# Performance work log

Measured on AMD Instinct MI355X. Metric: run time of the kernel, lower is better.

The kernel has to match this reference:

```python
import jax, jax.numpy as jnp
import numpy as np

B, P, D, A = 256, 196, 512, 512

def setup_inputs() -> dict:
    key = jax.random.key(0)
    ks = jax.random.split(key, 12)
    sc = 1.0 / np.sqrt(D)
    sa = 1.0 / np.sqrt(A)
    return {
        "encoder_out": jax.random.normal(ks[0], (B, P, D), jnp.float32),
        "decoder_hidden": jax.random.normal(ks[1], (B, D), jnp.float32),
        "st": jax.random.normal(ks[2], (B, D), jnp.float32),
        "Wv": jax.random.normal(ks[3], (D, A), jnp.float32) * sc,
        "bv": jnp.zeros((A,), jnp.float32),
        "Wh": jax.random.normal(ks[4], (D, A), jnp.float32) * sc,
        "bh": jnp.zeros((A,), jnp.float32),
        "Ws": jax.random.normal(ks[5], (D, A), jnp.float32) * sc,
        "bs": jnp.zeros((A,), jnp.float32),
        "Wav": jax.random.normal(ks[6], (A,), jnp.float32) * sa,
        "bav": jnp.zeros((), jnp.float32),
        "Was": jax.random.normal(ks[7], (A,), jnp.float32) * sa,
        "bas": jnp.zeros((), jnp.float32),
    }

def reference(encoder_out, decoder_hidden, st, Wv, bv, Wh, bh, Ws, bs, Wav, bav, Was, bas):
    # hidden: (B, A)
    hidden = decoder_hidden @ Wh + bh
    # v: (B, P, A)
    v = jnp.einsum('bpd,da->bpa', encoder_out, Wv) + bv
    # z_t: (B, P) -- additive attention scores over pixels
    z_t = jnp.einsum('bpa,a->bp', jnp.tanh(v + hidden[:, None, :]), Wav) + bav
    alpha_t = jax.nn.softmax(z_t, axis=1)
    # c_t: (B, D) -- attention-weighted encoding
    c_t = jnp.einsum('bpd,bp->bd', encoder_out, alpha_t)
    # sentinel branch: s (B, A), s_att (B, 1)
    s = st @ Ws + bs
    s_att = jnp.tanh(s + hidden) @ Was + bas  # (B,)
    z_t_extended = jnp.concatenate([z_t, s_att[:, None]], axis=1)  # (B, P+1)
    alpha_t_hat = jax.nn.softmax(z_t_extended, axis=1)
    beta_t = alpha_t_hat[:, -1:]  # (B, 1)
    c_hat_t = beta_t * st + (1.0 - beta_t) * c_t
    return (c_hat_t, alpha_t, beta_t)
```

## Files before the change

### kernel.cpp

```cpp
#include <hip/hip_runtime.h>
#include <hip/hip_bf16.h>
#include <cstdint>

#define B_ 256
#define P_ 196
#define D_ 512
#define A_ 512

#define OUT_CHAT  0
#define OUT_ALPHA (B_*D_)
#define OUT_BETA  (B_*D_ + B_*P_)

typedef unsigned short ushort_t;
typedef uint32_t u32;
typedef uint64_t u64;
typedef __attribute__((ext_vector_type(8))) __bf16 bf16x8;
typedef __attribute__((ext_vector_type(4))) float f32x4;

__device__ __forceinline__ ushort_t f2bf(float f) {
    union { float f; u32 i; } v; v.f = f;
    u32 r = (v.i + 0x7fffu + ((v.i >> 16) & 1u)) >> 16;
    return (ushort_t)r;
}
__device__ __forceinline__ u32 cvt2bf(float x, float y) {
    union { __hip_bfloat162 h; u32 u; } v;
    v.h = __float22bfloat162_rn(make_float2(x, y));
    return v.u;
}
__device__ __forceinline__ float tanh_fast(float x) {
    float e = __expf(2.0f * x);
    return 1.0f - 2.0f / (e + 1.0f);
}

__global__ __launch_bounds__(256) void k0_transpose(
    const float* __restrict__ W, ushort_t* __restrict__ WT)
{
    __shared__ ushort_t tile[32][33];
    int bx = blockIdx.x, by = blockIdx.y;
    int t = threadIdx.x, r = t >> 5, c = t & 31;
#pragma unroll
    for (int i = 0; i < 4; ++i) {
        int row = r + 8 * i;
        tile[row][c] = f2bf(W[(size_t)(by * 32 + row) * A_ + bx * 32 + c]);
    }
    __syncthreads();
#pragma unroll
    for (int i = 0; i < 4; ++i) {
        int row = r + 8 * i;
        WT[(size_t)(bx * 32 + row) * D_ + by * 32 + c] = tile[c][row];
    }
}

__global__ __launch_bounds__(256) void kcvt_small(
    const float* __restrict__ dh, const float* __restrict__ st,
    ushort_t* __restrict__ dhbf, ushort_t* __restrict__ stbf,
    float* __restrict__ z_ws, float* __restrict__ ct_ws)
{
    int gid = blockIdx.x * 256 + threadIdx.x;
    const float4* dsrc = (const float4*)dh;
    const float4* ssrc = (const float4*)st;
    float4 dv = dsrc[gid], sv = ssrc[gid];
    ((u64*)dhbf)[gid] = (u64)cvt2bf(dv.x, dv.y) | ((u64)cvt2bf(dv.z, dv.w) << 32);
    ((u64*)stbf)[gid] = (u64)cvt2bf(sv.x, sv.y) | ((u64)cvt2bf(sv.z, sv.w) << 32);
    ((float4*)ct_ws)[gid] = (float4){0.f, 0.f, 0.f, 0.f};
    z_ws[gid < B_ * P_ ? gid : 0] = 0.f;
    if (gid < B_ * P_ - 32768) z_ws[gid + 32768] = 0.f;
}

__global__ __launch_bounds__(256) void kE_cvt(
    const float* __restrict__ E, ushort_t* __restrict__ Ebf)
{
    size_t i0 = (size_t)blockIdx.x * 512 + threadIdx.x;
    const float4* src = (const float4*)E;
    u64* dst = (u64*)Ebf;
    float4 v0 = src[i0];
    float4 v1 = src[i0 + 256];
    u64 p0 = (u64)cvt2bf(v0.x, v0.y) | ((u64)cvt2bf(v0.z, v0.w) << 32);
    u64 p1 = (u64)cvt2bf(v1.x, v1.y) | ((u64)cvt2bf(v1.z, v1.w) << 32);
    dst[i0]       = p0;
    dst[i0 + 256] = p1;
}

#define PADK 72

__global__ __launch_bounds__(256) void k1_mfma(
    const ushort_t* __restrict__ dhbf, const ushort_t* __restrict__ stbf,
    const ushort_t* __restrict__ WhT,  const ushort_t* __restrict__ WsT,
    const float* __restrict__ bh, const float* __restrict__ bs,
    float* __restrict__ hidden_ws, float* __restrict__ s_ws)
{
    __shared__ ushort_t As[128 * PADK];
    __shared__ ushort_t Bs[128 * PADK];

    int mat = blockIdx.z;
    const ushort_t* Abf = mat ? stbf : dhbf;
    const ushort_t* WT  = mat ? WsT  : WhT;
    const float*    bia = mat ? bs   : bh;
    float*          outp = mat ? s_ws : hidden_ws;

    int tid = threadIdx.x;
    int m0 = blockIdx.y * 128;
    int n0 = blockIdx.x * 128;

    int lane = tid & 63, w = tid >> 6;
    int wm = w & 1, wn = w >> 1;
    int col = lane & 15, q = lane >> 4;

    f32x4 acc[4][4];
#pragma unroll
    for (int tm = 0; tm < 4; ++tm)
#pragma unroll
        for (int tn = 0; tn < 4; ++tn)
            acc[tm][tn] = (f32x4){0.f, 0.f, 0.f, 0.f};

    const ushort_t* arow = As + (wm * 64 + col) * PADK + q * 8;
    const ushort_t* brow = Bs + (wn * 64 + col) * PADK + q * 8;

    int sr = tid >> 3, sc = tid & 7;
    for (int kt = 0; kt < D_ / 64; ++kt) {
#pragma unroll
        for (int i = 0; i < 4; ++i) {
            int row = sr + i * 32;
            *(uint4*)(As + row * PADK + sc * 8) =
                *(const uint4*)(Abf + (size_t)(m0 + row) * D_ + kt * 64 + sc * 8);
            *(uint4*)(Bs + row * PADK + sc * 8) =
                *(const uint4*)(WT + (size_t)(n0 + row) * D_ + kt * 64 + sc * 8);
        }
        __syncthreads();
#pragma unroll
        for (int ks = 0; ks < 2; ++ks) {
            bf16x8 afr[4];
#pragma unroll
            for (int tm = 0; tm < 4; ++tm)
                afr[tm] = *(const bf16x8*)(arow + tm * 16 * PADK + ks * 32);
#pragma unroll
            for (int tn = 0; tn < 4; ++tn) {
                bf16x8 bfr = *(const bf16x8*)(brow + tn * 16 * PADK + ks * 32);
#pragma unroll
                for (int tm = 0; tm < 4; ++tm)
                    acc[tm][tn] = __builtin_amdgcn_mfma_f32_16x16x32_bf16(
                        afr[tm], bfr, acc[tm][tn], 0, 0, 0);
            }
        }
        __syncthreads();
    }

#pragma unroll
    for (int tm = 0; tm < 4; ++tm)
#pragma unroll
        for (int r = 0; r < 4; ++r) {
            int b = m0 + wm * 64 + tm * 16 + q * 4 + r;
#pragma unroll
            for (int tn = 0; tn < 4; ++tn) {
                int n = n0 + wn * 64 + tn * 16 + col;
                outp[(size_t)b * A_ + n] = acc[tm][tn][r] + bia[n];
            }
        }
}

#define BM 128
#define BN 256
#define BKk 64
__global__ __launch_bounds__(256, 2) void k2_z_bf(
    const ushort_t* __restrict__ Ebf, const ushort_t* __restrict__ WvT,
    const float* __restrict__ hidden_ws, const float* __restrict__ bv,
    const float* __restrict__ Wav, float* __restrict__ z_ws)
{
    __shared__ ushort_t As[BM * PADK];
    __shared__ ushort_t Bs[BN * PADK];
    __shared__ float hv_s[2][BN];
    __shared__ float wav_s[BN];
    __shared__ float zpart[2][BM];

    int tid = threadIdx.x;
    int m0  = blockIdx.x * BM;
    int n0  = blockIdx.y * BN;
    int b0  = m0 / P_;
    int b1  = (m0 + BM - 1) / P_;

    {
        int a = n0 + tid;
        float bva = bv[a];
        hv_s[0][tid] = hidden_ws[(size_t)b0 * A_ + a] + bva;
        hv_s[1][tid] = hidden_ws[(size_t)b1 * A_ + a] + bva;
        wav_s[tid]   = Wav[a];
    }

    int lane = tid & 63, w = tid >> 6;
    int wm = w & 1, wn = w >> 1;
    int col = lane & 15, q = lane >> 4;

    f32x4 acc[4][8];
#pragma unroll
    for (int tm = 0; tm < 4; ++tm)
#pragma unroll
        for (int tn = 0; tn < 8; ++tn)
            acc[tm][tn] = (f32x4){0.f, 0.f, 0.f, 0.f};

    const ushort_t* arow = As + (wm * 64 + col) * PADK + q * 8;
    const ushort_t* brow = Bs + (wn * 128 + col) * PADK + q * 8;

    int sr = tid >> 3, sc = tid & 7;

    for (int kt = 0; kt < D_ / BKk; ++kt) {
#pragma unroll
        for (int i = 0; i < 4; ++i) {
            int row = sr + i * 32;
            *(uint4*)(As + row * PADK + sc * 8) =
                *(const uint4*)(Ebf + (size_t)(m0 + row) * D_ + kt * BKk + sc * 8);
        }
#pragma unroll
        for (int i = 0; i < 8; ++i) {
            int row = sr + i * 32;
            *(uint4*)(Bs + row * PADK + sc * 8) =
                *(const uint4*)(WvT + (size_t)(n0 + row) * D_ + kt * BKk + sc * 8);
        }
        __syncthreads();
#pragma unroll
        for (int ks = 0; ks < 2; ++ks) {
            bf16x8 afr[4], bfr[8];
#pragma unroll
            for (int tm = 0; tm < 4; ++tm)
                afr[tm] = *(const bf16x8*)(arow + tm * 16 * PADK + ks * 32);
#pragma unroll
            for (int tn = 0; tn < 8; ++tn)
                bfr[tn] = *(const bf16x8*)(brow + tn * 16 * PADK + ks * 32);
#pragma unroll
            for (int tm = 0; tm < 4; ++tm)
#pragma unroll
                for (int tn = 0; tn < 8; ++tn)
                    acc[tm][tn] = __builtin_amdgcn_mfma_f32_16x16x32_bf16(
                        afr[tm], bfr[tn], acc[tm][tn], 0, 0, 0);
        }
        __syncthreads();
    }

#pragma unroll
    for (int tm = 0; tm < 4; ++tm) {
#pragma unroll
        for (int r = 0; r < 4; ++r) {
            int row = wm * 64 + tm * 16 + q * 4 + r;
            int m   = m0 + row;
            int bsel = (m / P_) - b0;
            float zr = 0.f;
#pragma unroll
            for (int tn = 0; tn < 8; ++tn) {
                int nl = wn * 128 + tn * 16 + col;
                zr += wav_s[nl] * tanh_fast(acc[tm][tn][r] + hv_s[bsel][nl]);
            }
#pragma unroll
            for (int msk = 1; msk < 16; msk <<= 1)
                zr += __shfl_xor(zr, msk, 64);
            if (col == 0) zpart[wn][row] = zr;
        }
    }
    __syncthreads();
    if (tid < BM) {
        int m = m0 + tid;
        int b = m / P_;
        int p = m - b * P_;
        atomicAdd(&z_ws[(size_t)b * P_ + p], zpart[0][tid] + zpart[1][tid]);
    }
}

__global__ __launch_bounds__(256) void k3_softmax(
    const float* __restrict__ z_ws, const float* __restrict__ hidden_ws,
    const float* __restrict__ s_ws, const float* __restrict__ Was,
    const float* __restrict__ bas, const float* __restrict__ bav,
    float* __restrict__ alpha_ws, float* __restrict__ beta_ws,
    float* __restrict__ out)
{
    __shared__ float red[4];
    __shared__ float bm_s, bl_s, sa_s;
    int b = blockIdx.x, t = threadIdx.x;

    {
        int a0 = t, a1 = t + 256;
        float part = Was[a0] * tanh_fast(s_ws[(size_t)b * A_ + a0] + hidden_ws[(size_t)b * A_ + a0])
                   + Was[a1] * tanh_fast(s_ws[(size_t)b * A_ + a1] + hidden_ws[(size_t)b * A_ + a1]);
#pragma unroll
        for (int o = 32; o >= 1; o >>= 1) part += __shfl_down(part, o, 64);
        if ((t & 63) == 0) red[t >> 6] = part;
        __syncthreads();
        if (t == 0) sa_s = red[0] + red[1] + red[2] + red[3] + bas[0];
        __syncthreads();
    }

    float zv = (t < P_) ? (z_ws[(size_t)b * P_ + t] + bav[0]) : -1e30f;

    float m = zv;
#pragma unroll
    for (int o = 32; o >= 1; o >>= 1) m = fmaxf(m, __shfl_xor(m, o, 64));
    if ((t & 63) == 0) red[t >> 6] = m;
    __syncthreads();
    if (t == 0) bm_s = fmaxf(fmaxf(red[0], red[1]), fmaxf(red[2], red[3]));
    __syncthreads();
    float m1 = bm_s;

    float e = (t < P_) ? __expf(zv - m1) : 0.f;
    float s = e;
#pragma unroll
    for (int o = 32; o >= 1; o >>= 1) s += __shfl_xor(s, o, 64);
    if ((t & 63) == 0) red[t >> 6] = s;
    __syncthreads();
    if (t == 0) bl_s = red[0] + red[1] + red[2] + red[3];
    __syncthreads();
    float l1 = bl_s;

    if (t < P_) {
        float alpha = e / l1;
        alpha_ws[(size_t)b * P_ + t] = alpha;
        out[OUT_ALPHA + (size_t)b * P_ + t] = alpha;
    }
    float sa = sa_s;
    float m2 = fmaxf(m1, sa);
    float l2 = __expf(m1 - m2) * l1 + __expf(sa - m2);
    float beta = __expf(sa - m2) / l2;
    if (t == 0) {
        beta_ws[b] = beta;
        out[OUT_BETA + b] = beta;
    }
}

#define PCH 49
__global__ __launch_bounds__(256) void k4_ct_partial(
    const float* __restrict__ E, const float* __restrict__ alpha_ws,
    float* __restrict__ ct_ws)
{
    __shared__ float al[PCH];
    int b = blockIdx.x, pc = blockIdx.y, t = threadIdx.x;
    int pbase = pc * PCH;
    if (t < PCH) al[t] = alpha_ws[(size_t)b * P_ + pbase + t];
    __syncthreads();
    const float* eb = E + ((size_t)b * P_ + pbase) * D_ + 2 * t;
    float a0 = 0.f, a1 = 0.f;
#pragma unroll 7
    for (int p = 0; p < PCH; ++p) {
        float2 u = *(const float2*)(eb + (size_t)p * D_);
        float ap = al[p];
        a0 = fmaf(ap, u.x, a0);
        a1 = fmaf(ap, u.y, a1);
    }
    atomicAdd(&ct_ws[(size_t)b * D_ + 2 * t],     a0);
    atomicAdd(&ct_ws[(size_t)b * D_ + 2 * t + 1], a1);
}

__global__ __launch_bounds__(256) void k4_combine(
    const float* __restrict__ st, const float* __restrict__ ct_ws,
    const float* __restrict__ beta_ws, float* __restrict__ out)
{
    int b = blockIdx.x, t = threadIdx.x;
    float beta = beta_ws[b];
    float2 su = *(const float2*)(st + (size_t)b * D_ + 2 * t);
    float2 cu = *(const float2*)(ct_ws + (size_t)b * D_ + 2 * t);
    float c0 = beta * su.x + (1.f - beta) * cu.x;
    float c1 = beta * su.y + (1.f - beta) * cu.y;
    *(float2*)(out + (size_t)b * D_ + 2 * t) = make_float2(c0, c1);
}

extern "C" void kernel_launch(void* const* d_in, const int* in_sizes, int n_in,
                              void* d_out, int out_size, void* d_ws, size_t ws_size,
                              hipStream_t stream)
{
    (void)in_sizes; (void)n_in; (void)out_size; (void)ws_size;
    const float* E   = (const float*)d_in[0];
    const float* dh  = (const float*)d_in[1];
    const float* st  = (const float*)d_in[2];
    const float* Wv  = (const float*)d_in[3];
    const float* bv  = (const float*)d_in[4];
    const float* Wh  = (const float*)d_in[5];
    const float* bh  = (const float*)d_in[6];
    const float* Ws  = (const float*)d_in[7];
    const float* bs  = (const float*)d_in[8];
    const float* Wav = (const float*)d_in[9];
    const float* bav = (const float*)d_in[10];
    const float* Was = (const float*)d_in[11];
    const float* bas = (const float*)d_in[12];
    float* out = (float*)d_out;

    char* ws = (char*)d_ws;
    ushort_t* WvT      = (ushort_t*)(ws);
    ushort_t* WhT      = (ushort_t*)(ws + 524288);
    ushort_t* WsT      = (ushort_t*)(ws + 1048576);
    float*    hidden_w = (float*)(ws + 1572864);
    float*    s_w      = (float*)(ws + 2097152);
    float*    z_w      = (float*)(ws + 2621440);
    float*    alpha_w  = (float*)(ws + 2822144);
    float*    beta_w   = (float*)(ws + 3022848);
    float*    ct_w     = (float*)(ws + 3023872);
    ushort_t* dhbf     = (ushort_t*)(ws + 3548160);
    ushort_t* stbf     = (ushort_t*)(ws + 3810304);
    ushort_t* Ebf      = (ushort_t*)(ws + 4072448);

    k0_transpose<<<dim3(16, 16), 256, 0, stream>>>(Wv, WvT);
    k0_transpose<<<dim3(16, 16), 256, 0, stream>>>(Wh, WhT);
    k0_transpose<<<dim3(16, 16), 256, 0, stream>>>(Ws, WsT);
    kcvt_small<<<128, 256, 0, stream>>>(dh, st, dhbf, stbf, z_w, ct_w);
    kE_cvt<<<(B_ * P_ * D_) / 4 / 512, 256, 0, stream>>>(E, Ebf);
    k1_mfma<<<dim3(4, 2, 2), 256, 0, stream>>>(dhbf, stbf, WhT, WsT, bh, bs,
                                               hidden_w, s_w);
    k2_z_bf<<<dim3((B_ * P_) / BM, A_ / BN), 256, 0, stream>>>(
        Ebf, WvT, hidden_w, bv, Wav, z_w);
    k3_softmax<<<256, 256, 0, stream>>>(z_w, hidden_w, s_w, Was, bas, bav,
                                        alpha_w, beta_w, out);
    k4_ct_partial<<<dim3(B_, P_ / PCH), 256, 0, stream>>>(E, alpha_w, ct_w);
    k4_combine<<<256, 256, 0, stream>>>(st, ct_w, beta_w, out);
}
```

Before: 274.1 us.

## Fuse prep kernels, async LDS loads with XOR swizzle, drop atomics in z and ctx

Merges the three weight transposes into one launch and folds the small activation conversions into the big E-conversion kernel, which also removes the zeroing pass. The main GEMM now loads tiles straight into LDS with global_load_lds and uses an XOR-swizzled unpadded layout instead of padded rows. Its occupancy hint rises from 2 to 3 blocks per CU. Atomic accumulation of z and c_t is replaced by per-split partial buffers that are summed downstream, with the context chunk size doubled. This trades fewer launches, no atomics and less register staging against extra partial reads and a reuse of workspace where ctp aliases hidden.

```diff
diff --git a/kernel.cpp b/kernel.cpp
--- a/kernel.cpp
+++ b/kernel.cpp
@@ -22,6 +22,9 @@
     u32 r = (v.i + 0x7fffu + ((v.i >> 16) & 1u)) >> 16;
     return (ushort_t)r;
 }
+__device__ __forceinline__ float bfbits2f(u32 lo16) {
+    union { u32 i; float f; } v; v.i = lo16 << 16; return v.f;
+}
 __device__ __forceinline__ u32 cvt2bf(float x, float y) {
     union { __hip_bfloat162 h; u32 u; } v;
     v.h = __float22bfloat162_rn(make_float2(x, y));
@@ -31,11 +34,21 @@
     float e = __expf(2.0f * x);
     return 1.0f - 2.0f / (e + 1.0f);
 }
-
-__global__ __launch_bounds__(256) void k0_transpose(
-    const float* __restrict__ W, ushort_t* __restrict__ WT)
+__device__ __forceinline__ void async_load16(const ushort_t* g, ushort_t* l) {
+    __builtin_amdgcn_global_load_lds(
+        (const __attribute__((address_space(1))) unsigned int*)g,
+        (__attribute__((address_space(3))) unsigned int*)l, 16, 0, 0);
+}
+
+__global__ __launch_bounds__(256) void k0_all(
+    const float* __restrict__ Wv, const float* __restrict__ Wh,
+    const float* __restrict__ Ws,
+    ushort_t* __restrict__ WvT, ushort_t* __restrict__ WhT,
+    ushort_t* __restrict__ WsT)
 {
     __shared__ ushort_t tile[32][33];
+    const float* W = (blockIdx.z == 0) ? Wv : (blockIdx.z == 1) ? Wh : Ws;
+    ushort_t*    WT = (blockIdx.z == 0) ? WvT : (blockIdx.z == 1) ? WhT : WsT;
     int bx = blockIdx.x, by = blockIdx.y;
     int t = threadIdx.x, r = t >> 5, c = t & 31;
 #pragma unroll
@@ -51,34 +64,28 @@
     }
 }
 
-__global__ __launch_bounds__(256) void kcvt_small(
-    const float* __restrict__ dh, const float* __restrict__ st,
-    ushort_t* __restrict__ dhbf, ushort_t* __restrict__ stbf,
-    float* __restrict__ z_ws, float* __restrict__ ct_ws)
-{
-    int gid = blockIdx.x * 256 + threadIdx.x;
-    const float4* dsrc = (const float4*)dh;
-    const float4* ssrc = (const float4*)st;
-    float4 dv = dsrc[gid], sv = ssrc[gid];
-    ((u64*)dhbf)[gid] = (u64)cvt2bf(dv.x, dv.y) | ((u64)cvt2bf(dv.z, dv.w) << 32);
-    ((u64*)stbf)[gid] = (u64)cvt2bf(sv.x, sv.y) | ((u64)cvt2bf(sv.z, sv.w) << 32);
-    ((float4*)ct_ws)[gid] = (float4){0.f, 0.f, 0.f, 0.f};
-    z_ws[gid < B_ * P_ ? gid : 0] = 0.f;
-    if (gid < B_ * P_ - 32768) z_ws[gid + 32768] = 0.f;
-}
-
-__global__ __launch_bounds__(256) void kE_cvt(
-    const float* __restrict__ E, ushort_t* __restrict__ Ebf)
-{
-    size_t i0 = (size_t)blockIdx.x * 512 + threadIdx.x;
-    const float4* src = (const float4*)E;
-    u64* dst = (u64*)Ebf;
-    float4 v0 = src[i0];
-    float4 v1 = src[i0 + 256];
-    u64 p0 = (u64)cvt2bf(v0.x, v0.y) | ((u64)cvt2bf(v0.z, v0.w) << 32);
-    u64 p1 = (u64)cvt2bf(v1.x, v1.y) | ((u64)cvt2bf(v1.z, v1.w) << 32);
-    dst[i0]       = p0;
-    dst[i0 + 256] = p1;
+__global__ __launch_bounds__(256) void kE_plus(
+    const float* __restrict__ E, const float* __restrict__ dh,
+    const float* __restrict__ st,
+    ushort_t* __restrict__ Ebf, ushort_t* __restrict__ dhbf,
+    ushort_t* __restrict__ stbf)
+{
+    int bx = blockIdx.x;
+    if (bx < 12544) {
+        size_t i0 = (size_t)bx * 512 + threadIdx.x;
+        const float4* src = (const float4*)E;
+        u64* dst = (u64*)Ebf;
+        float4 v0 = src[i0];
+        float4 v1 = src[i0 + 256];
+        dst[i0]       = (u64)cvt2bf(v0.x, v0.y) | ((u64)cvt2bf(v0.z, v0.w) << 32);
+        dst[i0 + 256] = (u64)cvt2bf(v1.x, v1.y) | ((u64)cvt2bf(v1.z, v1.w) << 32);
+    } else {
+        int gid = (bx - 12544) * 256 + threadIdx.x;
+        float4 dv = ((const float4*)dh)[gid];
+        float4 sv = ((const float4*)st)[gid];
+        ((u64*)dhbf)[gid] = (u64)cvt2bf(dv.x, dv.y) | ((u64)cvt2bf(dv.z, dv.w) << 32);
+        ((u64*)stbf)[gid] = (u64)cvt2bf(sv.x, sv.y) | ((u64)cvt2bf(sv.z, sv.w) << 32);
+    }
 }
 
 #define PADK 72
@@ -161,13 +168,13 @@
 #define BM 128
 #define BN 256
 #define BKk 64
-__global__ __launch_bounds__(256, 2) void k2_z_bf(
+__global__ __launch_bounds__(256, 3) void k2_z_bf(
     const ushort_t* __restrict__ Ebf, const ushort_t* __restrict__ WvT,
     const float* __restrict__ hidden_ws, const float* __restrict__ bv,
-    const float* __restrict__ Wav, float* __restrict__ z_ws)
-{
-    __shared__ ushort_t As[BM * PADK];
-    __shared__ ushort_t Bs[BN * PADK];
+    const float* __restrict__ Wav, float* __restrict__ z2_ws)
+{
+    __shared__ ushort_t As[BM * BKk];
+    __shared__ ushort_t Bs[BN * BKk];
     __shared__ float hv_s[2][BN];
     __shared__ float wav_s[BN];
     __shared__ float zpart[2][BM];
@@ -197,40 +204,39 @@
         for (int tn = 0; tn < 8; ++tn)
             acc[tm][tn] = (f32x4){0.f, 0.f, 0.f, 0.f};
 
-    const ushort_t* arow = As + (wm * 64 + col) * PADK + q * 8;
-    const ushort_t* brow = Bs + (wn * 128 + col) * PADK + q * 8;
-
-    int sr = tid >> 3, sc = tid & 7;
+    int srow = tid >> 3, spos = tid & 7;
+    int gch  = spos ^ (srow & 7);
+    const ushort_t* agb = Ebf + (size_t)(m0 + srow) * D_ + gch * 8;
+    const ushort_t* bgb = WvT + (size_t)(n0 + srow) * D_ + gch * 8;
+    ushort_t* alb = As + tid * 8;
+    ushort_t* blb = Bs + tid * 8;
+
+    int fx = col & 7;
 
     for (int kt = 0; kt < D_ / BKk; ++kt) {
 #pragma unroll
-        for (int i = 0; i < 4; ++i) {
-            int row = sr + i * 32;
-            *(uint4*)(As + row * PADK + sc * 8) =
-                *(const uint4*)(Ebf + (size_t)(m0 + row) * D_ + kt * BKk + sc * 8);
-        }
-#pragma unroll
-        for (int i = 0; i < 8; ++i) {
-            int row = sr + i * 32;
-            *(uint4*)(Bs + row * PADK + sc * 8) =
-                *(const uint4*)(WvT + (size_t)(n0 + row) * D_ + kt * BKk + sc * 8);
-        }
+        for (int i = 0; i < 4; ++i)
+            async_load16(agb + (size_t)i * 32 * D_ + kt * BKk, alb + i * 2048);
+#pragma unroll
+        for (int i = 0; i < 8; ++i)
+            async_load16(bgb + (size_t)i * 32 * D_ + kt * BKk, blb + i * 2048);
         __syncthreads();
 #pragma unroll
         for (int ks = 0; ks < 2; ++ks) {
-            bf16x8 afr[4], bfr[8];
+            bf16x8 afr[4];
 #pragma unroll
             for (int tm = 0; tm < 4; ++tm)
-                afr[tm] = *(const bf16x8*)(arow + tm * 16 * PADK + ks * 32);
-#pragma unroll
-            for (int tn = 0; tn < 8; ++tn)
-                bfr[tn] = *(const bf16x8*)(brow + tn * 16 * PADK + ks * 32);
-#pragma unroll
-            for (int tm = 0; tm < 4; ++tm)
-#pragma unroll
-                for (int tn = 0; tn < 8; ++tn)
+                afr[tm] = *(const bf16x8*)(As + (wm * 64 + tm * 16 + col) * BKk
+                                              + (((ks * 4 + q) ^ fx) * 8));
+#pragma unroll
+            for (int tn = 0; tn < 8; ++tn) {
+                bf16x8 bfr = *(const bf16x8*)(Bs + (wn * 128 + tn * 16 + col) * BKk
+                                                 + (((ks * 4 + q) ^ fx) * 8));
+#pragma unroll
+                for (int tm = 0; tm < 4; ++tm)
                     acc[tm][tn] = __builtin_amdgcn_mfma_f32_16x16x32_bf16(
-                        afr[tm], bfr[tn], acc[tm][tn], 0, 0, 0);
+                        afr[tm], bfr, acc[tm][tn], 0, 0, 0);
+            }
         }
         __syncthreads();
     }
@@ -255,16 +261,13 @@
         }
     }
     __syncthreads();
-    if (tid < BM) {
-        int m = m0 + tid;
-        int b = m / P_;
-        int p = m - b * P_;
-        atomicAdd(&z_ws[(size_t)b * P_ + p], zpart[0][tid] + zpart[1][tid]);
-    }
+    if (tid < BM)
+        z2_ws[(size_t)blockIdx.y * (B_ * P_) + m0 + tid] =
+            zpart[0][tid] + zpart[1][tid];
 }
 
 __global__ __launch_bounds__(256) void k3_softmax(
-    const float* __restrict__ z_ws, const float* __restrict__ hidden_ws,
+    const float* __restrict__ z2_ws, const float* __restrict__ hidden_ws,
     const float* __restrict__ s_ws, const float* __restrict__ Was,
     const float* __restrict__ bas, const float* __restrict__ bav,
     float* __restrict__ alpha_ws, float* __restrict__ beta_ws,
@@ -286,7 +289,9 @@
         __syncthreads();
     }
 
-    float zv = (t < P_) ? (z_ws[(size_t)b * P_ + t] + bav[0]) : -1e30f;
+    float zv = (t < P_) ? (z2_ws[(size_t)b * P_ + t]
+                         + z2_ws[(size_t)(B_ * P_) + (size_t)b * P_ + t] + bav[0])
+                        : -1e30f;
 
     float m = zv;
 #pragma unroll
@@ -322,10 +327,10 @@
     }
 }
 
-#define PCH 49
+#define PCH 98
 __global__ __launch_bounds__(256) void k4_ct_partial(
     const float* __restrict__ E, const float* __restrict__ alpha_ws,
-    float* __restrict__ ct_ws)
+    float* __restrict__ ctp)
 {
     __shared__ float al[PCH];
     int b = blockIdx.x, pc = blockIdx.y, t = threadIdx.x;
@@ -341,20 +346,20 @@
         a0 = fmaf(ap, u.x, a0);
         a1 = fmaf(ap, u.y, a1);
     }
-    atomicAdd(&ct_ws[(size_t)b * D_ + 2 * t],     a0);
-    atomicAdd(&ct_ws[(size_t)b * D_ + 2 * t + 1], a1);
+    *(float2*)(ctp + ((size_t)pc * B_ + b) * D_ + 2 * t) = make_float2(a0, a1);
 }
 
 __global__ __launch_bounds__(256) void k4_combine(
-    const float* __restrict__ st, const float* __restrict__ ct_ws,
+    const float* __restrict__ st, const float* __restrict__ ctp,
     const float* __restrict__ beta_ws, float* __restrict__ out)
 {
     int b = blockIdx.x, t = threadIdx.x;
     float beta = beta_ws[b];
     float2 su = *(const float2*)(st + (size_t)b * D_ + 2 * t);
-    float2 cu = *(const float2*)(ct_ws + (size_t)b * D_ + 2 * t);
-    float c0 = beta * su.x + (1.f - beta) * cu.x;
-    float c1 = beta * su.y + (1.f - beta) * cu.y;
+    float2 c0v = *(const float2*)(ctp + (size_t)b * D_ + 2 * t);
+    float2 c1v = *(const float2*)(ctp + ((size_t)B_ + b) * D_ + 2 * t);
+    float c0 = beta * su.x + (1.f - beta) * (c0v.x + c1v.x);
+    float c1 = beta * su.y + (1.f - beta) * (c0v.y + c1v.y);
     *(float2*)(out + (size_t)b * D_ + 2 * t) = make_float2(c0, c1);
 }
 
@@ -379,30 +384,27 @@
     float* out = (float*)d_out;
 
     char* ws = (char*)d_ws;
-    ushort_t* WvT      = (ushort_t*)(ws);
-    ushort_t* WhT      = (ushort_t*)(ws + 524288);
-    ushort_t* WsT      = (ushort_t*)(ws + 1048576);
-    float*    hidden_w = (float*)(ws + 1572864);
-    float*    s_w      = (float*)(ws + 2097152);
-    float*    z_w      = (float*)(ws + 2621440);
-    float*    alpha_w  = (float*)(ws + 2822144);
-    float*    beta_w   = (float*)(ws + 3022848);
-    float*    ct_w     = (float*)(ws + 3023872);
-    ushort_t* dhbf     = (ushort_t*)(ws + 3548160);
-    ushort_t* stbf     = (ushort_t*)(ws + 3810304);
-    ushort_t* Ebf      = (ushort_t*)(ws + 4072448);
-
-    k0_transpose<<<dim3(16, 16), 256, 0, stream>>>(Wv, WvT);
-    k0_transpose<<<dim3(16, 16), 256, 0, stream>>>(Wh, WhT);
-    k0_transpose<<<dim3(16, 16), 256, 0, stream>>>(Ws, WsT);
-    kcvt_small<<<128, 256, 0, stream>>>(dh, st, dhbf, stbf, z_w, ct_w);
-    kE_cvt<<<(B_ * P_ * D_) / 4 / 512, 256, 0, stream>>>(E, Ebf);
+    ushort_t* WvT     = (ushort_t*)(ws);
+    ushort_t* WhT     = (ushort_t*)(ws + 524288);
+    ushort_t* WsT     = (ushort_t*)(ws + 1048576);
+    float*    alpha_w = (float*)(ws + 1572864);
+    float*    beta_w  = (float*)(ws + 1773568);
+    float*    z2_w    = (float*)(ws + 1774592);
+    ushort_t* dhbf    = (ushort_t*)(ws + 2176000);
+    ushort_t* stbf    = (ushort_t*)(ws + 2438144);
+    float*    hidden_w= (float*)(ws + 2700288);
+    float*    s_w     = (float*)(ws + 3224576);
+    float*    ctp_w   = (float*)(ws + 2700288);
+    ushort_t* Ebf     = (ushort_t*)(ws + 3748864);
+
+    k0_all<<<dim3(16, 16, 3), 256, 0, stream>>>(Wv, Wh, Ws, WvT, WhT, WsT);
+    kE_plus<<<12544 + 128, 256, 0, stream>>>(E, dh, st, Ebf, dhbf, stbf);
     k1_mfma<<<dim3(4, 2, 2), 256, 0, stream>>>(dhbf, stbf, WhT, WsT, bh, bs,
                                                hidden_w, s_w);
     k2_z_bf<<<dim3((B_ * P_) / BM, A_ / BN), 256, 0, stream>>>(
-        Ebf, WvT, hidden_w, bv, Wav, z_w);
-    k3_softmax<<<256, 256, 0, stream>>>(z_w, hidden_w, s_w, Was, bas, bav,
+        Ebf, WvT, hidden_w, bv, Wav, z2_w);
+    k3_softmax<<<256, 256, 0, stream>>>(z2_w, hidden_w, s_w, Was, bas, bav,
                                         alpha_w, beta_w, out);
-    k4_ct_partial<<<dim3(B_, P_ / PCH), 256, 0, stream>>>(E, alpha_w, ct_w);
-    k4_combine<<<256, 256, 0, stream>>>(st, ct_w, beta_w, out);
-}
+    k4_ct_partial<<<dim3(B_, 2), 256, 0, stream>>>(E, alpha_w, ctp_w);
+    k4_combine<<<256, 256, 0, stream>>>(st, ctp_w, beta_w, out);
+}
```

Measured after the change: 261.9 us. 1.05x faster.
